# Performance work log

Measured on AMD Instinct MI355X. Metric: run time of the kernel, lower is better.

## Reference

```python
import jax, jax.numpy as jnp
import numpy as np

D_MODEL = 1024
D_STATE = 16
D_CONV = 4
EXPAND = 2
D_INNER = EXPAND * D_MODEL
DT_RANK = (D_MODEL + 15) // 16  # ceil(d_model/16) = 64
BATCH = 2
SEQLEN = 2048


def setup_inputs() -> dict:
    key = jax.random.key(0)
    ks = jax.random.split(key, 8)
    s = lambda k, shape, scale: jax.random.normal(k, shape, dtype=jnp.float32) * scale
    return {
        "x": s(ks[0], (BATCH, SEQLEN, D_MODEL), 1.0),
        "W_in": s(ks[1], (D_MODEL, 2 * D_INNER), D_MODEL ** -0.5),
        "conv_w": s(ks[2], (D_INNER, 1, D_CONV), 0.3),          # depthwise kernel (out, in/groups, k)
        "conv_b": jnp.zeros((D_INNER,), dtype=jnp.float32),
        "W_x": s(ks[3], (D_INNER, DT_RANK + 2 * D_STATE), D_INNER ** -0.5),
        "W_dt": s(ks[4], (DT_RANK, D_INNER), 2.0 * DT_RANK ** -0.5),  # uniform init std in torch; normal ok for reference
        "b_dt": s(ks[5], (D_INNER,), 0.1),
        "A_log": jnp.log(jnp.tile(jnp.arange(1, D_STATE + 1, dtype=jnp.float32), (D_INNER, 1))),
        "D": jnp.ones((D_INNER,), dtype=jnp.float32),
        "W_out": s(ks[6], (D_INNER, D_MODEL), D_INNER ** -0.5),
    }


def reference(x, W_in, conv_w, conv_b, W_x, W_dt, b_dt, A_log, D, W_out):
    dt_rank = W_dt.shape[0]
    d_state = A_log.shape[1]
    Bsz, L, _ = x.shape
    d_inner = conv_w.shape[0]

    # in_proj and split into x / res branches
    xr = x @ W_in                              # (B, L, 2*d_inner)
    xi, res = jnp.split(xr, 2, axis=-1)

    # causal depthwise conv1d: pad left by d_conv-1, truncate to L (same as torch pad+slice)
    xc = jax.lax.conv_general_dilated(
        xi.transpose(0, 2, 1),                 # (B, d_inner, L)
        conv_w,                                # (d_inner, 1, d_conv)
        window_strides=(1,),
        padding=[(conv_w.shape[-1] - 1, 0)],
        feature_group_count=d_inner,
    ) + conv_b[None, :, None]
    u = jax.nn.silu(xc.transpose(0, 2, 1))     # (B, L, d_inner)

    # x_proj -> delta_rank, B, C
    dbc = u @ W_x                              # (B, L, dt_rank + 2*d_state)
    delta_r = dbc[..., :dt_rank]
    Bm = dbc[..., dt_rank:dt_rank + d_state]   # (B, L, d_state)
    Cm = dbc[..., dt_rank + d_state:]          # (B, L, d_state)

    delta = jax.nn.softplus(delta_r @ W_dt + b_dt)   # (B, L, d_inner)
    A = -jnp.exp(A_log)                              # (d_inner, d_state)

    deltaA = jnp.exp(delta[..., None] * A)                           # (B, L, d_inner, d_state)
    dBu = delta[..., None] * Bm[:, :, None, :] * u[..., None]        # (B, L, d_inner, d_state)

    def step(h, inp):
        dA_t, dBu_t, C_t = inp
        h = dA_t * h + dBu_t                         # (B, d_inner, d_state)
        y_t = jnp.einsum('bdn,bn->bd', h, C_t)
        return h, y_t

    h0 = jnp.zeros((Bsz, d_inner, d_state), dtype=x.dtype)
    _, ys = jax.lax.scan(
        step, h0,
        (deltaA.transpose(1, 0, 2, 3), dBu.transpose(1, 0, 2, 3), Cm.transpose(1, 0, 2)),
    )
    y = ys.transpose(1, 0, 2) + u * D               # (B, L, d_inner)

    y = y * jax.nn.silu(res)
    return y @ W_out                                # (B, L, d_model)
```

## Files before the change

kernel.cpp:

```cpp
#include <hip/hip_runtime.h>

#define DM   1024
#define DI   2048
#define DSZ  16
#define DTR  64
#define BB   2
#define LL   2048
#define MM   (BB*LL)

using bfrag8 = __attribute__((ext_vector_type(8))) short;
using facc4  = __attribute__((ext_vector_type(4))) float;

__device__ __forceinline__ unsigned short f2bf(float f) {
  unsigned int u = __float_as_uint(f);
  u += 0x7fffu + ((u >> 16) & 1u);
  return (unsigned short)(u >> 16);
}

__device__ __forceinline__ float sigmoidf_(float x) { return 1.f / (1.f + __expf(-x)); }
__device__ __forceinline__ float softplusf_(float x) { return (x > 20.f) ? x : log1pf(__expf(x)); }

__device__ __forceinline__ void gload16(const void* g, void* l) {
  __builtin_amdgcn_global_load_lds(
      (__attribute__((address_space(1))) void*)(g),
      (__attribute__((address_space(3))) void*)(l), 16, 0, 0);
}


__global__ __launch_bounds__(256) void cvt_bf16(const float* __restrict__ s,
                                                unsigned short* __restrict__ d, int n) {
  int i = (blockIdx.x * 256 + threadIdx.x) * 4;
  if (i + 3 < n) {
    float4 v = *(const float4*)(s + i);
    ushort4 o;
    o.x = f2bf(v.x); o.y = f2bf(v.y); o.z = f2bf(v.z); o.w = f2bf(v.w);
    *(ushort4*)(d + i) = o;
  }
}

__global__ __launch_bounds__(256) void transpose_cvt(const float* __restrict__ src,
                                                     unsigned short* __restrict__ dst,
                                                     int R, int C) {
  __shared__ float tile[32][33];
  int c0 = blockIdx.x * 32, r0 = blockIdx.y * 32;
  for (int i = threadIdx.y; i < 32; i += 8)
    tile[i][threadIdx.x] = src[(size_t)(r0 + i) * C + c0 + threadIdx.x];
  __syncthreads();
  for (int i = threadIdx.y; i < 32; i += 8)
    dst[(size_t)(c0 + i) * R + r0 + threadIdx.x] = f2bf(tile[threadIdx.x][i]);
}

__global__ __launch_bounds__(256) void extract_dr(const float* __restrict__ dbc,
                                                  unsigned short* __restrict__ dr) {
  int i = blockIdx.x * 256 + threadIdx.x;
  if (i < MM * DTR) {
    int row = i >> 6, c = i & 63;
    dr[i] = f2bf(dbc[(size_t)row * 96 + c]);
  }
}

__global__ __launch_bounds__(256) void conv_silu(const float* __restrict__ xr,
                                                 const float* __restrict__ cw,
                                                 const float* __restrict__ cb,
                                                 float* __restrict__ uf,
                                                 unsigned short* __restrict__ ubf) {
  const int d = blockIdx.x * 256 + threadIdx.x;
  const int b = blockIdx.z;
  const int t0 = blockIdx.y * 64;
  const float w0 = cw[d * 4 + 0], w1 = cw[d * 4 + 1], w2 = cw[d * 4 + 2], w3 = cw[d * 4 + 3];
  const float bias = cb[d];
  const size_t base = ((size_t)b * LL) * (2 * DI) + d;
  float xm3 = (t0 >= 3) ? xr[base + (size_t)(t0 - 3) * (2 * DI)] : 0.f;
  float xm2 = (t0 >= 2) ? xr[base + (size_t)(t0 - 2) * (2 * DI)] : 0.f;
  float xm1 = (t0 >= 1) ? xr[base + (size_t)(t0 - 1) * (2 * DI)] : 0.f;
  for (int t = t0; t < t0 + 64; ++t) {
    float x0 = xr[base + (size_t)t * (2 * DI)];
    float a = bias + w0 * xm3 + w1 * xm2 + w2 * xm1 + w3 * x0;
    float uu = a * sigmoidf_(a);
    size_t oi = ((size_t)b * LL + t) * DI + d;
    uf[oi] = uu;
    ubf[oi] = f2bf(uu);
    xm3 = xm2; xm2 = xm1; xm1 = x0;
  }
}

template<int BM, int BN, int WMN, int WNN, int MF, int NF, int EPI>
__global__ __launch_bounds__(256, 2) void gemm_bf16(const unsigned short* __restrict__ A,
                                                    const unsigned short* __restrict__ Bt,
                                                    float* __restrict__ C,
                                                    const float* __restrict__ bias,
                                                    int M, int N, int K, int kLen) {
  static_assert(WMN * WNN == 4 && WMN * MF * 16 == BM && WNN * NF * 16 == BN, "geom");
  __shared__ unsigned short smem[(BM + BN) * 32];
  unsigned short* As = smem;
  unsigned short* Bs = smem + BM * 32;
  const int tid = threadIdx.x;
  const int wave = tid >> 6, lane = tid & 63;
  const int tM = blockIdx.y * BM, tN = blockIdx.x * BN;
  const int k0 = blockIdx.z * kLen;
  const int lrow = lane >> 2, lq = lane & 3;
  const int wm = wave / WNN, wn = wave % WNN;
  const int fr = lane & 15, kg = lane >> 4;

  facc4 acc[MF][NF];
#pragma unroll
  for (int mi = 0; mi < MF; ++mi)
#pragma unroll
    for (int ni = 0; ni < NF; ++ni)
#pragma unroll
      for (int r = 0; r < 4; ++r) acc[mi][ni][r] = 0.f;

  for (int kk = k0; kk < k0 + kLen; kk += 32) {
    __syncthreads();
    for (int r = wave; r < BM / 16; r += 4) {
      int row = r * 16 + lrow;
      int lcb = (lq ^ ((row >> 1) & 3)) << 4;
      const char* src = (const char*)(A + (size_t)(tM + row) * K + kk) + lcb;
      gload16(src, (char*)As + r * 1024);
    }
    for (int r = wave; r < BN / 16; r += 4) {
      int row = r * 16 + lrow;
      int lcb = (lq ^ ((row >> 1) & 3)) << 4;
      const char* src = (const char*)(Bt + (size_t)(tN + row) * K + kk) + lcb;
      gload16(src, (char*)Bs + r * 1024);
    }
    __syncthreads();

    bfrag8 af[MF], bfr[NF];
#pragma unroll
    for (int mi = 0; mi < MF; ++mi) {
      int row = wm * (MF * 16) + mi * 16 + fr;
      af[mi] = *(const bfrag8*)((const char*)As + row * 64 + ((kg ^ ((row >> 1) & 3)) << 4));
    }
#pragma unroll
    for (int ni = 0; ni < NF; ++ni) {
      int row = wn * (NF * 16) + ni * 16 + fr;
      bfr[ni] = *(const bfrag8*)((const char*)Bs + row * 64 + ((kg ^ ((row >> 1) & 3)) << 4));
    }
#pragma unroll
    for (int mi = 0; mi < MF; ++mi)
#pragma unroll
      for (int ni = 0; ni < NF; ++ni)
        acc[mi][ni] = __builtin_amdgcn_mfma_f32_16x16x32_bf16(af[mi], bfr[ni], acc[mi][ni], 0, 0, 0);
  }

  const int orow = tM + wm * (MF * 16), ocol = tN + wn * (NF * 16);
#pragma unroll
  for (int mi = 0; mi < MF; ++mi)
#pragma unroll
    for (int ni = 0; ni < NF; ++ni)
#pragma unroll
      for (int r = 0; r < 4; ++r) {
        int row = orow + mi * 16 + kg * 4 + r;
        int col = ocol + ni * 16 + fr;
        float v = acc[mi][ni][r];
        size_t idx = (size_t)row * N + col;
        if (EPI == 0)      C[idx] = v;
        else if (EPI == 1) C[idx] = softplusf_(v + bias[col]);
        else               atomicAdd(&C[idx], v);
      }
}

__global__ __launch_bounds__(256) void scan_kernel(const float* __restrict__ delta,
                                                   const float* __restrict__ dbc,
                                                   const float* __restrict__ u,
                                                   const float* __restrict__ xr,
                                                   const float* __restrict__ A_log,
                                                   const float* __restrict__ Dv,
                                                   unsigned short* __restrict__ ybf) {
  const int tid = threadIdx.x;
  const int ci = tid >> 4, n = tid & 15;
  const int lt = tid >> 4, lc = tid & 15;
  const int ch0 = blockIdx.x * 16;
  const int b = ch0 / DI;
  const int d0 = ch0 % DI;
  const float Adn = -__expf(A_log[(d0 + ci) * DSZ + n]);
  const float Dd = Dv[d0 + lc];
  __shared__ float sdel[2][16][16], su[2][16][16], sres[2][16][16], sB[2][16][16], sC[2][16][16];
  __shared__ float sp[16][16][20];
  const size_t rb = (size_t)b * LL;

  {
    const size_t row = rb + lt;
    sdel[0][lt][lc] = delta[row * DI + d0 + lc];
    su[0][lt][lc]   = u[row * DI + d0 + lc];
    sres[0][lt][lc] = xr[row * (2 * DI) + DI + d0 + lc];
    sB[0][lt][lc]   = dbc[row * 96 + DTR + lc];
    sC[0][lt][lc]   = dbc[row * 96 + DTR + DSZ + lc];
  }
  __syncthreads();

  float h = 0.f;
  const int nch = LL / 16;
  for (int c = 0; c < nch; ++c) {
    const int cur = c & 1;
    float r0 = 0, r1 = 0, r2 = 0, r3 = 0, r4 = 0;
    const bool nxt = (c + 1) < nch;
    if (nxt) {
      const size_t row = rb + (size_t)(c + 1) * 16 + lt;
      r0 = delta[row * DI + d0 + lc];
      r1 = u[row * DI + d0 + lc];
      r2 = xr[row * (2 * DI) + DI + d0 + lc];
      r3 = dbc[row * 96 + DTR + lc];
      r4 = dbc[row * 96 + DTR + DSZ + lc];
    }
#pragma unroll
    for (int tt = 0; tt < 16; ++tt) {
      float dl = sdel[cur][tt][ci];
      float uu = su[cur][tt][ci];
      float dA = __expf(dl * Adn);
      float dBu = dl * sB[cur][tt][n] * uu;
      h = __builtin_fmaf(dA, h, dBu);
      sp[tt][ci][n] = h * sC[cur][tt][n];
    }
    __syncthreads();
    {
      const facc4* p4 = (const facc4*)(&sp[lt][lc][0]);
      facc4 s0 = p4[0], s1 = p4[1], s2 = p4[2], s3 = p4[3];
      facc4 ss = s0 + s1 + s2 + s3;
      float ysum = ss.x + ss.y + ss.z + ss.w;
      float uu = su[cur][lt][lc];
      float rs = sres[cur][lt][lc];
      float yv = (ysum + uu * Dd) * (rs * sigmoidf_(rs));
      const size_t row = rb + (size_t)c * 16 + lt;
      ybf[row * DI + d0 + lc] = f2bf(yv);
    }
    if (nxt) {
      const int nb = cur ^ 1;
      sdel[nb][lt][lc] = r0; su[nb][lt][lc] = r1; sres[nb][lt][lc] = r2;
      sB[nb][lt][lc] = r3; sC[nb][lt][lc] = r4;
    }
    __syncthreads();
  }
}

extern "C" void kernel_launch(void* const* d_in, const int* in_sizes, int n_in,
                              void* d_out, int out_size, void* d_ws, size_t ws_size,
                              hipStream_t stream) {
  const float* x     = (const float*)d_in[0];
  const float* W_in  = (const float*)d_in[1];
  const float* convw = (const float*)d_in[2];
  const float* convb = (const float*)d_in[3];
  const float* W_x   = (const float*)d_in[4];
  const float* W_dt  = (const float*)d_in[5];
  const float* b_dt  = (const float*)d_in[6];
  const float* A_log = (const float*)d_in[7];
  const float* Dv    = (const float*)d_in[8];
  const float* W_out = (const float*)d_in[9];
  float* out = (float*)d_out;

  char* ws = (char*)d_ws;
  size_t off = 0;
  auto alloc = [&](size_t bytes) { char* p = ws + off; off += (bytes + 255) & ~(size_t)255; return p; };
  unsigned short* xbf   = (unsigned short*)alloc((size_t)MM * DM * 2);
  unsigned short* Wint  = (unsigned short*)alloc((size_t)(2 * DI) * DM * 2);
  float*          xr    = (float*)alloc((size_t)MM * (2 * DI) * 4);
  float*          uf    = (float*)alloc((size_t)MM * DI * 4);
  unsigned short* ubf   = (unsigned short*)alloc((size_t)MM * DI * 2);
  unsigned short* Wxt   = (unsigned short*)alloc((size_t)96 * DI * 2);
  float*          dbc   = (float*)alloc((size_t)MM * 96 * 4);
  unsigned short* drbf  = (unsigned short*)alloc((size_t)MM * DTR * 2);
  unsigned short* Wdtt  = (unsigned short*)alloc((size_t)DI * DTR * 2);
  float*          delta = (float*)alloc((size_t)MM * DI * 4);
  unsigned short* ybf   = (unsigned short*)alloc((size_t)MM * DI * 2);
  unsigned short* Woutt = (unsigned short*)alloc((size_t)DM * DI * 2);

  cvt_bf16<<<(MM * DM / 4) / 256, 256, 0, stream>>>(x, xbf, MM * DM);
  transpose_cvt<<<dim3((2 * DI) / 32, DM / 32), dim3(32, 8), 0, stream>>>(W_in, Wint, DM, 2 * DI);
  transpose_cvt<<<dim3(96 / 32, DI / 32), dim3(32, 8), 0, stream>>>(W_x, Wxt, DI, 96);
  transpose_cvt<<<dim3(DI / 32, DTR / 32), dim3(32, 8), 0, stream>>>(W_dt, Wdtt, DTR, DI);
  transpose_cvt<<<dim3(DM / 32, DI / 32), dim3(32, 8), 0, stream>>>(W_out, Woutt, DI, DM);

  gemm_bf16<128, 128, 2, 2, 4, 4, 0><<<dim3((2 * DI) / 128, MM / 128, 1), 256, 0, stream>>>(
      xbf, Wint, xr, nullptr, MM, 2 * DI, DM, DM);

  conv_silu<<<dim3(DI / 256, LL / 64, BB), 256, 0, stream>>>(xr, convw, convb, uf, ubf);

  hipMemsetAsync(dbc, 0, (size_t)MM * 96 * 4, stream);
  gemm_bf16<128, 96, 4, 1, 2, 6, 2><<<dim3(1, MM / 128, 8), 256, 0, stream>>>(
      ubf, Wxt, dbc, nullptr, MM, 96, DI, DI / 8);

  extract_dr<<<(MM * DTR) / 256, 256, 0, stream>>>(dbc, drbf);

  gemm_bf16<128, 128, 2, 2, 4, 4, 1><<<dim3(DI / 128, MM / 128, 1), 256, 0, stream>>>(
      drbf, Wdtt, delta, b_dt, MM, DI, DTR, DTR);

  scan_kernel<<<(BB * DI) / 16, 256, 0, stream>>>(delta, dbc, uf, xr, A_log, Dv, ybf);

  gemm_bf16<128, 128, 2, 2, 4, 4, 0><<<dim3(DM / 128, MM / 128, 1), 256, 0, stream>>>(
      ybf, Woutt, out, nullptr, MM, DM, DI, DI);
}
```

Baseline: 401.8 us.

## Split selective scan into segmented three-pass chunked scan across sequence

Replaces the single sequential scan kernel (256 blocks each walking all 2048 timesteps) with a three-pass segmented scan. Pass 1 computes per-segment decay products and partial states over 16 sequence segments, a small prefix kernel combines them into initial states, and pass 2 reruns each segment from its initial state to produce outputs. This gives 16x more blocks to fill the GPU and shortens the serial dependency chain. It also replaces the shared-memory reduction over state with wave shuffles. The cost is reading delta, u and B twice, plus two extra launches and a small state buffer.

```diff
diff --git a/kernel.cpp b/kernel.cpp
--- a/kernel.cpp
+++ b/kernel.cpp
@@ -7,6 +7,9 @@
 #define BB   2
 #define LL   2048
 #define MM   (BB*LL)
+#define SEG  16
+#define TSEG (LL/SEG)
+#define NCH  (BB*DI)
 
 using bfrag8 = __attribute__((ext_vector_type(8))) short;
 using facc4  = __attribute__((ext_vector_type(4))) float;
@@ -161,24 +164,96 @@
       }
 }
 
-__global__ __launch_bounds__(256) void scan_kernel(const float* __restrict__ delta,
-                                                   const float* __restrict__ dbc,
-                                                   const float* __restrict__ u,
-                                                   const float* __restrict__ xr,
-                                                   const float* __restrict__ A_log,
-                                                   const float* __restrict__ Dv,
-                                                   unsigned short* __restrict__ ybf) {
+__global__ __launch_bounds__(256) void scan_pass1(const float* __restrict__ delta,
+                                                  const float* __restrict__ dbc,
+                                                  const float* __restrict__ u,
+                                                  const float* __restrict__ A_log,
+                                                  float* __restrict__ pq) {
   const int tid = threadIdx.x;
   const int ci = tid >> 4, n = tid & 15;
-  const int lt = tid >> 4, lc = tid & 15;
+  const int lt = ci, lc = n;
   const int ch0 = blockIdx.x * 16;
-  const int b = ch0 / DI;
-  const int d0 = ch0 % DI;
+  const int b = ch0 / DI, d0 = ch0 % DI;
+  const int seg = blockIdx.y;
+  const float Adn = -__expf(A_log[(d0 + ci) * DSZ + n]);
+  __shared__ float sdel[2][16][16], su[2][16][16], sB[2][16][16];
+  const size_t rb = (size_t)b * LL + (size_t)seg * TSEG;
+
+  {
+    const size_t row = rb + lt;
+    sdel[0][lt][lc] = delta[row * DI + d0 + lc];
+    su[0][lt][lc]   = u[row * DI + d0 + lc];
+    sB[0][lt][lc]   = dbc[row * 96 + DTR + lc];
+  }
+  __syncthreads();
+
+  float h = 0.f, p = 1.f;
+  const int nch = TSEG / 16;
+  for (int c = 0; c < nch; ++c) {
+    const int cur = c & 1;
+    float r0 = 0, r1 = 0, r3 = 0;
+    const bool nxt = (c + 1) < nch;
+    if (nxt) {
+      const size_t row = rb + (size_t)(c + 1) * 16 + lt;
+      r0 = delta[row * DI + d0 + lc];
+      r1 = u[row * DI + d0 + lc];
+      r3 = dbc[row * 96 + DTR + lc];
+    }
+#pragma unroll
+    for (int tt = 0; tt < 16; ++tt) {
+      float dl = sdel[cur][tt][ci];
+      float uu = su[cur][tt][ci];
+      float dA = __expf(dl * Adn);
+      float dBu = dl * sB[cur][tt][n] * uu;
+      h = __builtin_fmaf(dA, h, dBu);
+      p *= dA;
+    }
+    if (nxt) {
+      const int nb = cur ^ 1;
+      sdel[nb][lt][lc] = r0; su[nb][lt][lc] = r1; sB[nb][lt][lc] = r3;
+    }
+    __syncthreads();
+  }
+  const size_t base = ((size_t)seg * NCH + ch0 + ci) * DSZ + n;
+  pq[base] = p;
+  pq[(size_t)SEG * NCH * DSZ + base] = h;
+}
+
+__global__ __launch_bounds__(256) void scan_prefix(const float* __restrict__ pq,
+                                                   float* __restrict__ hinit) {
+  const int i = blockIdx.x * 256 + threadIdx.x;
+  const size_t stride = (size_t)NCH * DSZ;
+  float h = 0.f;
+#pragma unroll
+  for (int s = 0; s < SEG; ++s) {
+    hinit[(size_t)s * stride + i] = h;
+    float P = pq[(size_t)s * stride + i];
+    float Q = pq[(size_t)SEG * stride + (size_t)s * stride + i];
+    h = __builtin_fmaf(P, h, Q);
+  }
+}
+
+__global__ __launch_bounds__(256) void scan_pass2(const float* __restrict__ delta,
+                                                  const float* __restrict__ dbc,
+                                                  const float* __restrict__ u,
+                                                  const float* __restrict__ xr,
+                                                  const float* __restrict__ A_log,
+                                                  const float* __restrict__ Dv,
+                                                  const float* __restrict__ hinit,
+                                                  unsigned short* __restrict__ ybf) {
+  const int tid = threadIdx.x;
+  const int ci = tid >> 4, n = tid & 15;
+  const int lt = ci, lc = n;
+  const int ch0 = blockIdx.x * 16;
+  const int b = ch0 / DI, d0 = ch0 % DI;
+  const int seg = blockIdx.y;
   const float Adn = -__expf(A_log[(d0 + ci) * DSZ + n]);
   const float Dd = Dv[d0 + lc];
   __shared__ float sdel[2][16][16], su[2][16][16], sres[2][16][16], sB[2][16][16], sC[2][16][16];
-  __shared__ float sp[16][16][20];
-  const size_t rb = (size_t)b * LL;
+  __shared__ float sy[16][16];
+  const size_t rb = (size_t)b * LL + (size_t)seg * TSEG;
+
+  float h = hinit[((size_t)seg * NCH + ch0 + ci) * DSZ + n];
 
   {
     const size_t row = rb + lt;
@@ -190,8 +265,7 @@
   }
   __syncthreads();
 
-  float h = 0.f;
-  const int nch = LL / 16;
+  const int nch = TSEG / 16;
   for (int c = 0; c < nch; ++c) {
     const int cur = c & 1;
     float r0 = 0, r1 = 0, r2 = 0, r3 = 0, r4 = 0;
@@ -211,14 +285,16 @@
       float dA = __expf(dl * Adn);
       float dBu = dl * sB[cur][tt][n] * uu;
       h = __builtin_fmaf(dA, h, dBu);
-      sp[tt][ci][n] = h * sC[cur][tt][n];
+      float py = h * sC[cur][tt][n];
+      py += __shfl_xor(py, 1, 16);
+      py += __shfl_xor(py, 2, 16);
+      py += __shfl_xor(py, 4, 16);
+      py += __shfl_xor(py, 8, 16);
+      if (n == 0) sy[tt][ci] = py;
     }
     __syncthreads();
     {
-      const facc4* p4 = (const facc4*)(&sp[lt][lc][0]);
-      facc4 s0 = p4[0], s1 = p4[1], s2 = p4[2], s3 = p4[3];
-      facc4 ss = s0 + s1 + s2 + s3;
-      float ysum = ss.x + ss.y + ss.z + ss.w;
+      float ysum = sy[lt][lc];
       float uu = su[cur][lt][lc];
       float rs = sres[cur][lt][lc];
       float yv = (ysum + uu * Dd) * (rs * sigmoidf_(rs));
@@ -264,6 +340,8 @@
   float*          delta = (float*)alloc((size_t)MM * DI * 4);
   unsigned short* ybf   = (unsigned short*)alloc((size_t)MM * DI * 2);
   unsigned short* Woutt = (unsigned short*)alloc((size_t)DM * DI * 2);
+  float*          pq    = (float*)alloc((size_t)2 * SEG * NCH * DSZ * 4);
+  float*          hinit = (float*)alloc((size_t)SEG * NCH * DSZ * 4);
 
   cvt_bf16<<<(MM * DM / 4) / 256, 256, 0, stream>>>(x, xbf, MM * DM);
   transpose_cvt<<<dim3((2 * DI) / 32, DM / 32), dim3(32, 8), 0, stream>>>(W_in, Wint, DM, 2 * DI);
@@ -285,7 +363,9 @@
   gemm_bf16<128, 128, 2, 2, 4, 4, 1><<<dim3(DI / 128, MM / 128, 1), 256, 0, stream>>>(
       drbf, Wdtt, delta, b_dt, MM, DI, DTR, DTR);
 
-  scan_kernel<<<(BB * DI) / 16, 256, 0, stream>>>(delta, dbc, uf, xr, A_log, Dv, ybf);
+  scan_pass1<<<dim3(NCH / 16, SEG), 256, 0, stream>>>(delta, dbc, uf, A_log, pq);
+  scan_prefix<<<(NCH * DSZ) / 256, 256, 0, stream>>>(pq, hinit);
+  scan_pass2<<<dim3(NCH / 16, SEG), 256, 0, stream>>>(delta, dbc, uf, xr, A_log, Dv, hinit, ybf);
 
   gemm_bf16<128, 128, 2, 2, 4, 4, 0><<<dim3(DM / 128, MM / 128, 1), 256, 0, stream>>>(
       ybf, Woutt, out, nullptr, MM, DM, DI, DI);
```

Measured after the change: 470.5 us. +17.1%, slower.

## Replace sequential selective scan with chunked three-pass parallel scan

Applied to the files above, without the earlier changes.

Replaces the single-pass scan, in which each block walks the whole 2048-step sequence for 16 channels, with a segmented scan. Pass one computes per-segment decay products and partial states, a prefix kernel combines the 32 segments, and pass two rescans each segment from its carried-in state while producing outputs. Each thread now holds all 16 state entries of one channel in registers, which removes the shared-memory reduction and barriers. This exposes 32x more parallelism along the sequence, at the cost of recomputing the exponentials twice and extra global traffic for the partial-state buffers.

```diff
diff --git a/kernel.cpp b/kernel.cpp
--- a/kernel.cpp
+++ b/kernel.cpp
@@ -7,6 +7,9 @@
 #define BB   2
 #define LL   2048
 #define MM   (BB*LL)
+#define SEG  32
+#define TSEG (LL/SEG)
+#define NCH  (BB*DI)
 
 using bfrag8 = __attribute__((ext_vector_type(8))) short;
 using facc4  = __attribute__((ext_vector_type(4))) float;
@@ -161,76 +164,113 @@
       }
 }
 
-__global__ __launch_bounds__(256) void scan_kernel(const float* __restrict__ delta,
-                                                   const float* __restrict__ dbc,
-                                                   const float* __restrict__ u,
-                                                   const float* __restrict__ xr,
-                                                   const float* __restrict__ A_log,
-                                                   const float* __restrict__ Dv,
-                                                   unsigned short* __restrict__ ybf) {
-  const int tid = threadIdx.x;
-  const int ci = tid >> 4, n = tid & 15;
-  const int lt = tid >> 4, lc = tid & 15;
-  const int ch0 = blockIdx.x * 16;
-  const int b = ch0 / DI;
-  const int d0 = ch0 % DI;
-  const float Adn = -__expf(A_log[(d0 + ci) * DSZ + n]);
-  const float Dd = Dv[d0 + lc];
-  __shared__ float sdel[2][16][16], su[2][16][16], sres[2][16][16], sB[2][16][16], sC[2][16][16];
-  __shared__ float sp[16][16][20];
-  const size_t rb = (size_t)b * LL;
-
+__global__ __launch_bounds__(256) void scan_pass1(const float* __restrict__ delta,
+                                                  const float* __restrict__ dbc,
+                                                  const float* __restrict__ u,
+                                                  const float* __restrict__ A_log,
+                                                  float* __restrict__ pq) {
+  const int b = blockIdx.x >> 3;
+  const int d = ((blockIdx.x & 7) << 8) | threadIdx.x;
+  const int ch = blockIdx.x * 256 + threadIdx.x;
+  const int seg = blockIdx.y;
+  const size_t rb = (size_t)b * LL + (size_t)seg * TSEG;
+  float A[DSZ], h[DSZ], P[DSZ];
+#pragma unroll
+  for (int n = 0; n < DSZ; ++n) {
+    A[n] = -__expf(A_log[d * DSZ + n]);
+    h[n] = 0.f;
+    P[n] = 1.f;
+  }
+  float dl = delta[rb * DI + d];
+  float uu = u[rb * DI + d];
+  for (int t = 0; t < TSEG; ++t) {
+    float dln = 0.f, uun = 0.f;
+    if (t + 1 < TSEG) {
+      dln = delta[(rb + t + 1) * DI + d];
+      uun = u[(rb + t + 1) * DI + d];
+    }
+    const float* Brow = dbc + (rb + t) * 96 + DTR;
+    const float dlu = dl * uu;
+#pragma unroll
+    for (int n = 0; n < DSZ; ++n) {
+      float dA = __expf(dl * A[n]);
+      h[n] = __builtin_fmaf(dA, h[n], dlu * Brow[n]);
+      P[n] *= dA;
+    }
+    dl = dln; uu = uun;
+  }
+  const size_t base = ((size_t)seg * NCH + ch) * DSZ;
+  float4* pP = (float4*)(pq + base);
+  float4* pQ = (float4*)(pq + (size_t)SEG * NCH * DSZ + base);
+#pragma unroll
+  for (int q = 0; q < 4; ++q) {
+    pP[q] = make_float4(P[4 * q], P[4 * q + 1], P[4 * q + 2], P[4 * q + 3]);
+    pQ[q] = make_float4(h[4 * q], h[4 * q + 1], h[4 * q + 2], h[4 * q + 3]);
+  }
+}
+
+__global__ __launch_bounds__(256) void scan_prefix(const float* __restrict__ pq,
+                                                   float* __restrict__ hinit) {
+  const int i = blockIdx.x * 256 + threadIdx.x;
+  const size_t stride = (size_t)NCH * DSZ;
+  float h = 0.f;
+#pragma unroll
+  for (int s = 0; s < SEG; ++s) {
+    hinit[(size_t)s * stride + i] = h;
+    float P = pq[(size_t)s * stride + i];
+    float Q = pq[(size_t)SEG * stride + (size_t)s * stride + i];
+    h = __builtin_fmaf(P, h, Q);
+  }
+}
+
+__global__ __launch_bounds__(256) void scan_pass2(const float* __restrict__ delta,
+                                                  const float* __restrict__ dbc,
+                                                  const float* __restrict__ u,
+                                                  const float* __restrict__ xr,
+                                                  const float* __restrict__ A_log,
+                                                  const float* __restrict__ Dv,
+                                                  const float* __restrict__ hinit,
+                                                  unsigned short* __restrict__ ybf) {
+  const int b = blockIdx.x >> 3;
+  const int d = ((blockIdx.x & 7) << 8) | threadIdx.x;
+  const int ch = blockIdx.x * 256 + threadIdx.x;
+  const int seg = blockIdx.y;
+  const size_t rb = (size_t)b * LL + (size_t)seg * TSEG;
+  float A[DSZ], h[DSZ];
+#pragma unroll
+  for (int n = 0; n < DSZ; ++n) A[n] = -__expf(A_log[d * DSZ + n]);
   {
-    const size_t row = rb + lt;
-    sdel[0][lt][lc] = delta[row * DI + d0 + lc];
-    su[0][lt][lc]   = u[row * DI + d0 + lc];
-    sres[0][lt][lc] = xr[row * (2 * DI) + DI + d0 + lc];
-    sB[0][lt][lc]   = dbc[row * 96 + DTR + lc];
-    sC[0][lt][lc]   = dbc[row * 96 + DTR + DSZ + lc];
-  }
-  __syncthreads();
-
-  float h = 0.f;
-  const int nch = LL / 16;
-  for (int c = 0; c < nch; ++c) {
-    const int cur = c & 1;
-    float r0 = 0, r1 = 0, r2 = 0, r3 = 0, r4 = 0;
-    const bool nxt = (c + 1) < nch;
-    if (nxt) {
-      const size_t row = rb + (size_t)(c + 1) * 16 + lt;
-      r0 = delta[row * DI + d0 + lc];
-      r1 = u[row * DI + d0 + lc];
-      r2 = xr[row * (2 * DI) + DI + d0 + lc];
-      r3 = dbc[row * 96 + DTR + lc];
-      r4 = dbc[row * 96 + DTR + DSZ + lc];
-    }
-#pragma unroll
-    for (int tt = 0; tt < 16; ++tt) {
-      float dl = sdel[cur][tt][ci];
-      float uu = su[cur][tt][ci];
-      float dA = __expf(dl * Adn);
-      float dBu = dl * sB[cur][tt][n] * uu;
-      h = __builtin_fmaf(dA, h, dBu);
-      sp[tt][ci][n] = h * sC[cur][tt][n];
-    }
-    __syncthreads();
-    {
-      const facc4* p4 = (const facc4*)(&sp[lt][lc][0]);
-      facc4 s0 = p4[0], s1 = p4[1], s2 = p4[2], s3 = p4[3];
-      facc4 ss = s0 + s1 + s2 + s3;
-      float ysum = ss.x + ss.y + ss.z + ss.w;
-      float uu = su[cur][lt][lc];
-      float rs = sres[cur][lt][lc];
-      float yv = (ysum + uu * Dd) * (rs * sigmoidf_(rs));
-      const size_t row = rb + (size_t)c * 16 + lt;
-      ybf[row * DI + d0 + lc] = f2bf(yv);
-    }
-    if (nxt) {
-      const int nb = cur ^ 1;
-      sdel[nb][lt][lc] = r0; su[nb][lt][lc] = r1; sres[nb][lt][lc] = r2;
-      sB[nb][lt][lc] = r3; sC[nb][lt][lc] = r4;
-    }
-    __syncthreads();
+    const float4* hp = (const float4*)(hinit + ((size_t)seg * NCH + ch) * DSZ);
+#pragma unroll
+    for (int q = 0; q < 4; ++q) {
+      float4 v = hp[q];
+      h[4 * q] = v.x; h[4 * q + 1] = v.y; h[4 * q + 2] = v.z; h[4 * q + 3] = v.w;
+    }
+  }
+  const float Dd = Dv[d];
+  float dl = delta[rb * DI + d];
+  float uu = u[rb * DI + d];
+  float rs = xr[rb * (2 * DI) + DI + d];
+  for (int t = 0; t < TSEG; ++t) {
+    float dln = 0.f, uun = 0.f, rsn = 0.f;
+    if (t + 1 < TSEG) {
+      dln = delta[(rb + t + 1) * DI + d];
+      uun = u[(rb + t + 1) * DI + d];
+      rsn = xr[(rb + t + 1) * (2 * DI) + DI + d];
+    }
+    const float* Brow = dbc + (rb + t) * 96 + DTR;
+    const float* Crow = Brow + DSZ;
+    const float dlu = dl * uu;
+    float y = 0.f;
+#pragma unroll
+    for (int n = 0; n < DSZ; ++n) {
+      float dA = __expf(dl * A[n]);
+      h[n] = __builtin_fmaf(dA, h[n], dlu * Brow[n]);
+      y = __builtin_fmaf(h[n], Crow[n], y);
+    }
+    float yv = (y + uu * Dd) * (rs * sigmoidf_(rs));
+    ybf[(rb + t) * DI + d] = f2bf(yv);
+    dl = dln; uu = uun; rs = rsn;
   }
 }
 
@@ -264,6 +304,8 @@
   float*          delta = (float*)alloc((size_t)MM * DI * 4);
   unsigned short* ybf   = (unsigned short*)alloc((size_t)MM * DI * 2);
   unsigned short* Woutt = (unsigned short*)alloc((size_t)DM * DI * 2);
+  float*          pq    = (float*)alloc((size_t)2 * SEG * NCH * DSZ * 4);
+  float*          hinit = (float*)alloc((size_t)SEG * NCH * DSZ * 4);
 
   cvt_bf16<<<(MM * DM / 4) / 256, 256, 0, stream>>>(x, xbf, MM * DM);
   transpose_cvt<<<dim3((2 * DI) / 32, DM / 32), dim3(32, 8), 0, stream>>>(W_in, Wint, DM, 2 * DI);
@@ -285,7 +327,9 @@
   gemm_bf16<128, 128, 2, 2, 4, 4, 1><<<dim3(DI / 128, MM / 128, 1), 256, 0, stream>>>(
       drbf, Wdtt, delta, b_dt, MM, DI, DTR, DTR);
 
-  scan_kernel<<<(BB * DI) / 16, 256, 0, stream>>>(delta, dbc, uf, xr, A_log, Dv, ybf);
+  scan_pass1<<<dim3(NCH / 256, SEG), 256, 0, stream>>>(delta, dbc, uf, A_log, pq);
+  scan_prefix<<<(NCH * DSZ) / 256, 256, 0, stream>>>(pq, hinit);
+  scan_pass2<<<dim3(NCH / 256, SEG), 256, 0, stream>>>(delta, dbc, uf, xr, A_log, Dv, hinit, ybf);
 
   gemm_bf16<128, 128, 2, 2, 4, 4, 0><<<dim3(DM / 128, MM / 128, 1), 256, 0, stream>>>(
       ybf, Woutt, out, nullptr, MM, DM, DI, DI);
```

New measurement: 405.6 us. About the same (+0.9%).
